# Optimization experiments

Measured on AMD Instinct MI355X. Metric: run time of the kernel, lower is better.

Reference implementation:

```python
import jax, jax.numpy as jnp
import numpy as np

VOCAB = 100000
DIM = 128
B = 16384
K = 20


def setup_inputs() -> dict:
    key = jax.random.key(0)
    k1, k2, k3, k4, k5 = jax.random.split(key, 5)
    return {
        "target": jax.random.randint(k1, (B,), 0, VOCAB),
        "context": jax.random.randint(k2, (B,), 0, VOCAB),
        "neg_samples": jax.random.randint(k3, (B, K), 0, VOCAB),
        "in_embed": jax.random.normal(k4, (VOCAB, DIM), dtype=jnp.float32),
        "out_embed": jax.random.normal(k5, (VOCAB, DIM), dtype=jnp.float32),
    }


def reference(target, context, neg_samples, in_embed, out_embed):
    t = in_embed[target]            # [B, D]
    c = out_embed[context]          # [B, D]
    n = out_embed[neg_samples]      # [B, K, D]

    pos_score = jnp.einsum("bd,bd->b", t, c)          # [B]
    pos_loss = jax.nn.log_sigmoid(pos_score)           # [B]

    neg_score = jnp.einsum("bd,bkd->bk", t, n)        # [B, K]
    neg_loss = jax.nn.log_sigmoid(-neg_score).sum(axis=1)  # [B]

    # Original torch broadcasts pos_loss[B] + neg_loss[B,1] -> [B,B] then .mean();
    # that equals mean(pos_loss) + mean(neg_loss), computed here without the [B,B].
    return -(pos_loss.mean() + neg_loss.mean())
```

## Files before the change

kernel.cpp:

```cpp
#include <hip/hip_runtime.h>
#include <hip/hip_bf16.h>

#define VOCAB 100000
#define DIM   128
#define BATCH 16384
#define KNEG  20

__global__ __launch_bounds__(256) void skipgram_loss_kernel(
    const int*   __restrict__ target,
    const int*   __restrict__ context,
    const int*   __restrict__ neg_samples,
    const float* __restrict__ in_embed,
    const float* __restrict__ out_embed,
    float*       __restrict__ out)
{
    const int lane  = threadIdx.x & 63;
    const int wave  = threadIdx.x >> 6;
    const int wpb   = blockDim.x >> 6;
    const int gwave = blockIdx.x * wpb + wave;
    const int nwav  = gridDim.x * wpb;

    float acc = 0.0f;

    for (int b = gwave; b < BATCH; b += nwav) {
        const int trow = target[b];
        const int crow = context[b];

        const float2 t2 = *(const float2*)(in_embed  + (size_t)trow * DIM + lane * 2);
        const float2 c2 = *(const float2*)(out_embed + (size_t)crow * DIM + lane * 2);

        float p[KNEG + 1];
        p[0] = t2.x * c2.x + t2.y * c2.y;

        #pragma unroll
        for (int k = 0; k < KNEG; ++k) {
            const int nrow = neg_samples[b * KNEG + k];
            const float2 n2 = *(const float2*)(out_embed + (size_t)nrow * DIM + lane * 2);
            p[k + 1] = t2.x * n2.x + t2.y * n2.y;
        }

        #pragma unroll
        for (int k = 0; k < KNEG + 1; ++k) {
            float v = p[k];
            #pragma unroll
            for (int m = 1; m < 64; m <<= 1)
                v += __shfl_xor(v, m, 64);
            const float x  = (k == 0) ? v : -v;
            const float ls = fminf(x, 0.0f) - __logf(1.0f + __expf(-fabsf(x)));
            acc += ls;
        }
    }

    __shared__ float smem[8];
    if (lane == 0) smem[wave] = acc;
    __syncthreads();
    if (threadIdx.x == 0) {
        float tot = 0.0f;
        for (int w = 0; w < wpb; ++w) tot += smem[w];
        atomicAdd(out, -tot * (1.0f / (float)BATCH));
    }
}

extern "C" void kernel_launch(void* const* d_in, const int* in_sizes, int n_in,
                              void* d_out, int out_size, void* d_ws, size_t ws_size,
                              hipStream_t stream) {
    const int*   target      = (const int*)  d_in[0];
    const int*   context     = (const int*)  d_in[1];
    const int*   neg_samples = (const int*)  d_in[2];
    const float* in_embed    = (const float*)d_in[3];
    const float* out_embed   = (const float*)d_in[4];
    float*       out         = (float*)d_out;

    hipMemsetAsync(out, 0, sizeof(float), stream);

    skipgram_loss_kernel<<<1024, 256, 0, stream>>>(
        target, context, neg_samples, in_embed, out_embed, out);
}
```

Before: 141.6 us.

## Map each batch row to a 16-lane group with float4 gathers

Each batch row is now handled by a 16-lane subgroup instead of a whole 64-lane wave. Each lane loads two float4 chunks per embedding row, and all negative indices are prefetched up front. The grid-stride loop is gone: each block covers exactly 16 rows, so the unchanged 1024-block launch covers the batch. This cuts the per-score shuffle reduction from six steps to four and puts all gathers for a row in flight at once, trading more registers per thread (also bounded via launch_bounds) for more memory-level parallelism.

```diff
diff --git a/kernel.cpp b/kernel.cpp
--- a/kernel.cpp
+++ b/kernel.cpp
@@ -1,12 +1,11 @@
 #include <hip/hip_runtime.h>
-#include <hip/hip_bf16.h>
 
 #define VOCAB 100000
 #define DIM   128
 #define BATCH 16384
 #define KNEG  20
 
-__global__ __launch_bounds__(256) void skipgram_loss_kernel(
+__global__ __launch_bounds__(256, 4) void skipgram_loss_kernel(
     const int*   __restrict__ target,
     const int*   __restrict__ context,
     const int*   __restrict__ neg_samples,
@@ -14,49 +13,59 @@
     const float* __restrict__ out_embed,
     float*       __restrict__ out)
 {
-    const int lane  = threadIdx.x & 63;
-    const int wave  = threadIdx.x >> 6;
-    const int wpb   = blockDim.x >> 6;
-    const int gwave = blockIdx.x * wpb + wave;
-    const int nwav  = gridDim.x * wpb;
+    const int tid  = threadIdx.x;
+    const int lane = tid & 63;
+    const int wave = tid >> 6;
+    const int g    = lane & 15;
+    const int b    = (blockIdx.x << 4) | (tid >> 4);
+
+    const int trow = target[b];
+    const int crow = context[b];
+
+    const float4* tp = (const float4*)(in_embed + (size_t)trow * DIM);
+    const float4  t0 = tp[g];
+    const float4  t1 = tp[16 + g];
+
+    int idx[KNEG];
+    #pragma unroll
+    for (int k = 0; k < KNEG; ++k) idx[k] = neg_samples[b * KNEG + k];
+
+    float p[KNEG + 1];
+    {
+        const float4* cp = (const float4*)(out_embed + (size_t)crow * DIM);
+        const float4 c0 = cp[g], c1 = cp[16 + g];
+        p[0] = t0.x*c0.x + t0.y*c0.y + t0.z*c0.z + t0.w*c0.w
+             + t1.x*c1.x + t1.y*c1.y + t1.z*c1.z + t1.w*c1.w;
+    }
+
+    #pragma unroll
+    for (int k = 0; k < KNEG; ++k) {
+        const float4* np = (const float4*)(out_embed + (size_t)idx[k] * DIM);
+        const float4 n0 = np[g], n1 = np[16 + g];
+        p[k + 1] = t0.x*n0.x + t0.y*n0.y + t0.z*n0.z + t0.w*n0.w
+                 + t1.x*n1.x + t1.y*n1.y + t1.z*n1.z + t1.w*n1.w;
+    }
 
     float acc = 0.0f;
-
-    for (int b = gwave; b < BATCH; b += nwav) {
-        const int trow = target[b];
-        const int crow = context[b];
-
-        const float2 t2 = *(const float2*)(in_embed  + (size_t)trow * DIM + lane * 2);
-        const float2 c2 = *(const float2*)(out_embed + (size_t)crow * DIM + lane * 2);
-
-        float p[KNEG + 1];
-        p[0] = t2.x * c2.x + t2.y * c2.y;
-
-        #pragma unroll
-        for (int k = 0; k < KNEG; ++k) {
-            const int nrow = neg_samples[b * KNEG + k];
-            const float2 n2 = *(const float2*)(out_embed + (size_t)nrow * DIM + lane * 2);
-            p[k + 1] = t2.x * n2.x + t2.y * n2.y;
-        }
-
-        #pragma unroll
-        for (int k = 0; k < KNEG + 1; ++k) {
-            float v = p[k];
-            #pragma unroll
-            for (int m = 1; m < 64; m <<= 1)
-                v += __shfl_xor(v, m, 64);
-            const float x  = (k == 0) ? v : -v;
-            const float ls = fminf(x, 0.0f) - __logf(1.0f + __expf(-fabsf(x)));
-            acc += ls;
-        }
+    #pragma unroll
+    for (int k = 0; k < KNEG + 1; ++k) {
+        float v = p[k];
+        v += __shfl_xor(v, 1, 64);
+        v += __shfl_xor(v, 2, 64);
+        v += __shfl_xor(v, 4, 64);
+        v += __shfl_xor(v, 8, 64);
+        const float x = (k == 0) ? v : -v;
+        acc += fminf(x, 0.0f) - __logf(1.0f + __expf(-fabsf(x)));
     }
 
-    __shared__ float smem[8];
+    acc += __shfl_xor(acc, 16, 64);
+    acc += __shfl_xor(acc, 32, 64);
+
+    __shared__ float smem[4];
     if (lane == 0) smem[wave] = acc;
     __syncthreads();
-    if (threadIdx.x == 0) {
-        float tot = 0.0f;
-        for (int w = 0; w < wpb; ++w) tot += smem[w];
+    if (tid == 0) {
+        const float tot = smem[0] + smem[1] + smem[2] + smem[3];
         atomicAdd(out, -tot * (1.0f / (float)BATCH));
     }
 }
```

New measurement: 138.4 us. 2.3% less time.
